# Kernel tuning notes

Measured on AMD Instinct MI355X. Metric: run time of the kernel, lower is better.

Reference implementation:

```python
import jax, jax.numpy as jnp
import numpy as np
from functools import reduce

# 2x2 beamsplitter gate (1/sqrt(2)) * [[1, i], [i, 1]]
BS_2x2 = (1.0 / np.sqrt(2.0)) * np.array([[1 + 0j, 0 + 1j], [0 + 1j, 1 + 0j]], dtype=np.complex64)


def _kron_phase_diag(a, b):
    """Diagonal vector of kron_i diag([e^{i a_i}, e^{i b_i}]) -> shape (2^n,) complex64.

    Mathematically identical to building the dense Kronecker diagonal matrix
    (as the original tf.linalg.LinearOperatorKronecker(...).to_dense()) and
    right-multiplying by it, since M @ diag(d) == M * d.
    """
    pairs = jnp.stack([jnp.exp(1j * a), jnp.exp(1j * b)], axis=1)  # (n, 2)
    n = pairs.shape[0]
    vec = pairs[0]
    for i in range(1, n):  # static small loop over qubits
        vec = jnp.kron(vec, pairs[i])
    return vec


def _bs_full(n):
    # Dense n-fold Kronecker product of the 2x2 beamsplitter, (2^n, 2^n) complex64
    return reduce(jnp.kron, [jnp.asarray(BS_2x2)] * n)


def setup_inputs() -> dict:
    key = jax.random.key(0)
    kx, ka, kb, kt, kp = jax.random.split(key, 5)
    n = 12
    N = 2 ** n
    batch = 64
    two_pi = 2.0 * np.pi
    return {
        "x": jax.random.normal(kx, (batch, 2, N), dtype=jnp.float32),
        "alphas": jax.random.uniform(ka, (n,), dtype=jnp.float32) * two_pi,
        "betas": jax.random.uniform(kb, (n,), dtype=jnp.float32) * two_pi,
        "thetas": jax.random.uniform(kt, (n,), dtype=jnp.float32) * two_pi,
        "phis": jax.random.uniform(kp, (n,), dtype=jnp.float32) * two_pi,
    }


def reference(x, alphas, betas, thetas, phis):
    n = alphas.shape[0]
    bs = _bs_full(n)                                   # (N, N) complex64
    d_in = _kron_phase_diag(alphas, betas)             # (N,)
    d_theta = _kron_phase_diag(thetas, jnp.zeros_like(thetas))
    d_phi = _kron_phase_diag(phis, jnp.zeros_like(phis))

    out = jax.lax.complex(x[:, 0, :], x[:, 1, :])      # (B, N) complex64
    out = (out * d_in) @ bs                            # input phase shifts + beamsplitter
    out = (out * d_theta) @ bs                         # theta shifts + beamsplitter
    out = out * d_phi                                  # final phi shifts
    return jnp.stack([out.real, out.imag], axis=1)     # (B, 2, N) float32
```

## Files before the change

kernel.cpp:

```cpp
#include <hip/hip_runtime.h>
#include <math.h>

#define NN 4096
#define BLK 512
#define EPT 8
#define PADSZ (NN + (NN >> 3))

__device__ __forceinline__ void cmul(float& ar, float& ai, float br, float bi) {
    float nr = ar * br - ai * bi;
    float ni = ar * bi + ai * br;
    ar = nr; ai = ni;
}

__device__ __forceinline__ void bfly_pair(float* vr, float* vi, int a, int b) {
    float ur = vr[a], ui = vi[a], wr = vr[b], wi = vi[b];
    vr[a] = ur - wi; vi[a] = ui + wr;
    vr[b] = wr - ui; vi[b] = wi + ur;
}

__device__ __forceinline__ void bfly3(float* vr, float* vi) {
    bfly_pair(vr, vi, 0, 1); bfly_pair(vr, vi, 2, 3); bfly_pair(vr, vi, 4, 5); bfly_pair(vr, vi, 6, 7);
    bfly_pair(vr, vi, 0, 2); bfly_pair(vr, vi, 1, 3); bfly_pair(vr, vi, 4, 6); bfly_pair(vr, vi, 5, 7);
    bfly_pair(vr, vi, 0, 4); bfly_pair(vr, vi, 1, 5); bfly_pair(vr, vi, 2, 6); bfly_pair(vr, vi, 3, 7);
}

template<int P>
__device__ __forceinline__ int jidx(int t, int r) {
    return ((t >> P) << (P + 3)) | (r << P) | (t & ((1 << P) - 1));
}

template<int PC, int PN, bool CROSS>
__device__ __forceinline__ void exchange(float2* buf, float* vr, float* vi, int t) {
    #pragma unroll
    for (int r = 0; r < EPT; ++r) {
        int j = jidx<PC>(t, r);
        buf[j + (j >> 3)] = make_float2(vr[r], vi[r]);
    }
    if (CROSS) { __syncthreads(); }
    else       { asm volatile("" ::: "memory"); }
    #pragma unroll
    for (int r = 0; r < EPT; ++r) {
        int j = jidx<PN>(t, r);
        float2 v = buf[j + (j >> 3)];
        vr[r] = v.x; vi[r] = v.y;
    }
}

__global__ __launch_bounds__(BLK) void qubit_layer_kernel(
    const float* __restrict__ x,
    const float* __restrict__ alphas, const float* __restrict__ betas,
    const float* __restrict__ thetas, const float* __restrict__ phis,
    float* __restrict__ out)
{
    __shared__ float2 B1[PADSZ];
    __shared__ float2 B2[PADSZ];
    __shared__ float2 tbl[6][64];

    const int t = threadIdx.x;
    const int b = blockIdx.x;

    if (t < 384) {
        int part = t >> 6, idx = t & 63, set = part >> 1, half = part & 1;
        float a = 0.f;
        #pragma unroll
        for (int m = 0; m < 6; ++m) {
            int q = half ? m : (6 + m);
            int bit = (idx >> (5 - m)) & 1;
            float av, bv;
            if (set == 0)      { av = alphas[q]; bv = betas[q]; }
            else if (set == 1) { av = thetas[q]; bv = 0.f; }
            else               { av = phis[q];   bv = 0.f; }
            a += bit ? bv : av;
        }
        float s, c;
        __sincosf(a, &s, &c);
        float sc = (set >= 1 && half == 0) ? (1.0f / 64.0f) : 1.0f;
        tbl[part][idx] = make_float2(c * sc, s * sc);
    }

    const float* xr = x + (size_t)b * 2 * NN;
    const float* xi = xr + NN;
    float vr[EPT], vi[EPT];
    {
        float4 a0 = ((const float4*)(xr + t * EPT))[0];
        float4 a1 = ((const float4*)(xr + t * EPT))[1];
        float4 c0 = ((const float4*)(xi + t * EPT))[0];
        float4 c1 = ((const float4*)(xi + t * EPT))[1];
        vr[0]=a0.x; vr[1]=a0.y; vr[2]=a0.z; vr[3]=a0.w; vr[4]=a1.x; vr[5]=a1.y; vr[6]=a1.z; vr[7]=a1.w;
        vi[0]=c0.x; vi[1]=c0.y; vi[2]=c0.z; vi[3]=c0.w; vi[4]=c1.x; vi[5]=c1.y; vi[6]=c1.z; vi[7]=c1.w;
    }
    __syncthreads();

    {
        float2 eh = tbl[1][t >> 3];
        const float4* elv = (const float4*)&tbl[0][(t & 7) << 3];
        #pragma unroll
        for (int k = 0; k < 4; ++k) {
            float4 e2 = elv[k];
            float er0 = e2.x, ei0 = e2.y, er1 = e2.z, ei1 = e2.w;
            cmul(er0, ei0, eh.x, eh.y);
            cmul(er1, ei1, eh.x, eh.y);
            cmul(vr[2*k],   vi[2*k],   er0, ei0);
            cmul(vr[2*k+1], vi[2*k+1], er1, ei1);
        }
    }

    bfly3(vr, vi);
    exchange<0, 3, false>(B1, vr, vi, t); bfly3(vr, vi);
    exchange<3, 6, false>(B1, vr, vi, t); bfly3(vr, vi);
    exchange<6, 9, true >(B1, vr, vi, t); bfly3(vr, vi);

    {
        float2 el = tbl[2][t & 63];
        #pragma unroll
        for (int r = 0; r < EPT; ++r) {
            float2 eh = tbl[3][(t >> 6) + (r << 3)];
            float er = el.x, ei = el.y;
            cmul(er, ei, eh.x, eh.y);
            cmul(vr[r], vi[r], er, ei);
        }
    }

    bfly3(vr, vi);
    exchange<9, 6, true >(B2, vr, vi, t); bfly3(vr, vi);
    exchange<6, 3, false>(B1, vr, vi, t); bfly3(vr, vi);
    exchange<3, 0, false>(B1, vr, vi, t); bfly3(vr, vi);

    {
        float2 eh = tbl[5][t >> 3];
        const float4* elv = (const float4*)&tbl[4][(t & 7) << 3];
        #pragma unroll
        for (int k = 0; k < 4; ++k) {
            float4 e2 = elv[k];
            float er0 = e2.x, ei0 = e2.y, er1 = e2.z, ei1 = e2.w;
            cmul(er0, ei0, eh.x, eh.y);
            cmul(er1, ei1, eh.x, eh.y);
            cmul(vr[2*k],   vi[2*k],   er0, ei0);
            cmul(vr[2*k+1], vi[2*k+1], er1, ei1);
        }
    }
    float* outr = out + (size_t)b * 2 * NN;
    float* outi = outr + NN;
    {
        ((float4*)(outr + t * EPT))[0] = make_float4(vr[0], vr[1], vr[2], vr[3]);
        ((float4*)(outr + t * EPT))[1] = make_float4(vr[4], vr[5], vr[6], vr[7]);
        ((float4*)(outi + t * EPT))[0] = make_float4(vi[0], vi[1], vi[2], vi[3]);
        ((float4*)(outi + t * EPT))[1] = make_float4(vi[4], vi[5], vi[6], vi[7]);
    }
}

extern "C" void kernel_launch(void* const* d_in, const int* in_sizes, int n_in,
                              void* d_out, int out_size, void* d_ws, size_t ws_size,
                              hipStream_t stream) {
    const float* x      = (const float*)d_in[0];
    const float* alphas = (const float*)d_in[1];
    const float* betas  = (const float*)d_in[2];
    const float* thetas = (const float*)d_in[3];
    const float* phis   = (const float*)d_in[4];
    float* out = (float*)d_out;

    const int batch = in_sizes[0] / (2 * NN);
    qubit_layer_kernel<<<batch, BLK, 0, stream>>>(x, alphas, betas, thetas, phis, out);
}
```

Before: 10.26 us.

## Replace LDS exchanges with wavefront shuffles and one XOR-swizzled transpose per transform

```diff
diff --git a/kernel.cpp b/kernel.cpp
--- a/kernel.cpp
+++ b/kernel.cpp
@@ -4,7 +4,6 @@
 #define NN 4096
 #define BLK 512
 #define EPT 8
-#define PADSZ (NN + (NN >> 3))
 
 __device__ __forceinline__ void cmul(float& ar, float& ai, float br, float bi) {
     float nr = ar * br - ai * bi;
@@ -24,26 +23,27 @@
     bfly_pair(vr, vi, 0, 4); bfly_pair(vr, vi, 1, 5); bfly_pair(vr, vi, 2, 6); bfly_pair(vr, vi, 3, 7);
 }
 
-template<int P>
-__device__ __forceinline__ int jidx(int t, int r) {
-    return ((t >> P) << (P + 3)) | (r << P) | (t & ((1 << P) - 1));
+__device__ __forceinline__ void shfl_stage(float* vr, float* vi, int mask) {
+    float pr[EPT], pi[EPT];
+    #pragma unroll
+    for (int r = 0; r < EPT; ++r) {
+        pr[r] = __shfl_xor(vr[r], mask);
+        pi[r] = __shfl_xor(vi[r], mask);
+    }
+    #pragma unroll
+    for (int r = 0; r < EPT; ++r) {
+        vr[r] -= pi[r];
+        vi[r] += pr[r];
+    }
 }
 
-template<int PC, int PN, bool CROSS>
-__device__ __forceinline__ void exchange(float2* buf, float* vr, float* vi, int t) {
-    #pragma unroll
-    for (int r = 0; r < EPT; ++r) {
-        int j = jidx<PC>(t, r);
-        buf[j + (j >> 3)] = make_float2(vr[r], vi[r]);
-    }
-    if (CROSS) { __syncthreads(); }
-    else       { asm volatile("" ::: "memory"); }
-    #pragma unroll
-    for (int r = 0; r < EPT; ++r) {
-        int j = jidx<PN>(t, r);
-        float2 v = buf[j + (j >> 3)];
-        vr[r] = v.x; vi[r] = v.y;
-    }
+__device__ __forceinline__ void shfl6(float* vr, float* vi) {
+    shfl_stage(vr, vi, 1);
+    shfl_stage(vr, vi, 2);
+    shfl_stage(vr, vi, 4);
+    shfl_stage(vr, vi, 8);
+    shfl_stage(vr, vi, 16);
+    shfl_stage(vr, vi, 32);
 }
 
 __global__ __launch_bounds__(BLK) void qubit_layer_kernel(
@@ -52,12 +52,21 @@
     const float* __restrict__ thetas, const float* __restrict__ phis,
     float* __restrict__ out)
 {
-    __shared__ float2 B1[PADSZ];
-    __shared__ float2 B2[PADSZ];
+    __shared__ float2 E1[NN];
+    __shared__ float2 E2[NN];
     __shared__ float2 tbl[6][64];
 
-    const int t = threadIdx.x;
-    const int b = blockIdx.x;
+    const int t   = threadIdx.x;
+    const int w   = t >> 6;
+    const int lam = t & 63;
+    const int b   = blockIdx.x;
+
+    const float* xr = x + (size_t)b * 2 * NN;
+    const float* xi = xr + NN;
+    float4 a0 = ((const float4*)(xr + t * EPT))[0];
+    float4 a1 = ((const float4*)(xr + t * EPT))[1];
+    float4 c0 = ((const float4*)(xi + t * EPT))[0];
+    float4 c1 = ((const float4*)(xi + t * EPT))[1];
 
     if (t < 384) {
         int part = t >> 6, idx = t & 63, set = part >> 1, half = part & 1;
@@ -78,22 +87,15 @@
         tbl[part][idx] = make_float2(c * sc, s * sc);
     }
 
-    const float* xr = x + (size_t)b * 2 * NN;
-    const float* xi = xr + NN;
     float vr[EPT], vi[EPT];
-    {
-        float4 a0 = ((const float4*)(xr + t * EPT))[0];
-        float4 a1 = ((const float4*)(xr + t * EPT))[1];
-        float4 c0 = ((const float4*)(xi + t * EPT))[0];
-        float4 c1 = ((const float4*)(xi + t * EPT))[1];
-        vr[0]=a0.x; vr[1]=a0.y; vr[2]=a0.z; vr[3]=a0.w; vr[4]=a1.x; vr[5]=a1.y; vr[6]=a1.z; vr[7]=a1.w;
-        vi[0]=c0.x; vi[1]=c0.y; vi[2]=c0.z; vi[3]=c0.w; vi[4]=c1.x; vi[5]=c1.y; vi[6]=c1.z; vi[7]=c1.w;
-    }
+    vr[0]=a0.x; vr[1]=a0.y; vr[2]=a0.z; vr[3]=a0.w; vr[4]=a1.x; vr[5]=a1.y; vr[6]=a1.z; vr[7]=a1.w;
+    vi[0]=c0.x; vi[1]=c0.y; vi[2]=c0.z; vi[3]=c0.w; vi[4]=c1.x; vi[5]=c1.y; vi[6]=c1.z; vi[7]=c1.w;
+
     __syncthreads();
 
     {
-        float2 eh = tbl[1][t >> 3];
-        const float4* elv = (const float4*)&tbl[0][(t & 7) << 3];
+        float2 eh = tbl[1][(w << 3) | (lam >> 3)];
+        const float4* elv = (const float4*)&tbl[0][(lam & 7) << 3];
         #pragma unroll
         for (int k = 0; k < 4; ++k) {
             float4 e2 = elv[k];
@@ -106,15 +108,25 @@
     }
 
     bfly3(vr, vi);
-    exchange<0, 3, false>(B1, vr, vi, t); bfly3(vr, vi);
-    exchange<3, 6, false>(B1, vr, vi, t); bfly3(vr, vi);
-    exchange<6, 9, true >(B1, vr, vi, t); bfly3(vr, vi);
+    shfl6(vr, vi);
+    {
+        #pragma unroll
+        for (int r = 0; r < EPT; ++r)
+            E1[(lam << 6) | (((w << 3) | r) ^ lam)] = make_float2(vr[r], vi[r]);
+        __syncthreads();
+        #pragma unroll
+        for (int r = 0; r < EPT; ++r) {
+            float2 v = E1[(lam << 6) | (((r << 3) | w) ^ lam)];
+            vr[r] = v.x; vi[r] = v.y;
+        }
+    }
+    bfly3(vr, vi);
 
     {
-        float2 el = tbl[2][t & 63];
+        float2 el = tbl[2][((lam & 7) << 3) | w];
         #pragma unroll
         for (int r = 0; r < EPT; ++r) {
-            float2 eh = tbl[3][(t >> 6) + (r << 3)];
+            float2 eh = tbl[3][(r << 3) | (lam >> 3)];
             float er = el.x, ei = el.y;
             cmul(er, ei, eh.x, eh.y);
             cmul(vr[r], vi[r], er, ei);
@@ -122,13 +134,23 @@
     }
 
     bfly3(vr, vi);
-    exchange<9, 6, true >(B2, vr, vi, t); bfly3(vr, vi);
-    exchange<6, 3, false>(B1, vr, vi, t); bfly3(vr, vi);
-    exchange<3, 0, false>(B1, vr, vi, t); bfly3(vr, vi);
+    shfl6(vr, vi);
+    {
+        #pragma unroll
+        for (int r = 0; r < EPT; ++r)
+            E2[(lam << 6) | (((r << 3) | w) ^ lam)] = make_float2(vr[r], vi[r]);
+        __syncthreads();
+        #pragma unroll
+        for (int r = 0; r < EPT; ++r) {
+            float2 v = E2[(lam << 6) | (((w << 3) | r) ^ lam)];
+            vr[r] = v.x; vi[r] = v.y;
+        }
+    }
+    bfly3(vr, vi);
 
     {
-        float2 eh = tbl[5][t >> 3];
-        const float4* elv = (const float4*)&tbl[4][(t & 7) << 3];
+        float2 eh = tbl[5][(w << 3) | (lam >> 3)];
+        const float4* elv = (const float4*)&tbl[4][(lam & 7) << 3];
         #pragma unroll
         for (int k = 0; k < 4; ++k) {
             float4 e2 = elv[k];
@@ -141,12 +163,10 @@
     }
     float* outr = out + (size_t)b * 2 * NN;
     float* outi = outr + NN;
-    {
-        ((float4*)(outr + t * EPT))[0] = make_float4(vr[0], vr[1], vr[2], vr[3]);
-        ((float4*)(outr + t * EPT))[1] = make_float4(vr[4], vr[5], vr[6], vr[7]);
-        ((float4*)(outi + t * EPT))[0] = make_float4(vi[0], vi[1], vi[2], vi[3]);
-        ((float4*)(outi + t * EPT))[1] = make_float4(vi[4], vi[5], vi[6], vi[7]);
-    }
+    ((float4*)(outr + t * EPT))[0] = make_float4(vr[0], vr[1], vr[2], vr[3]);
+    ((float4*)(outr + t * EPT))[1] = make_float4(vr[4], vr[5], vr[6], vr[7]);
+    ((float4*)(outi + t * EPT))[0] = make_float4(vi[0], vi[1], vi[2], vi[3]);
+    ((float4*)(outi + t * EPT))[1] = make_float4(vi[4], vi[5], vi[6], vi[7]);
 }
 
 extern "C" void kernel_launch(void* const* d_in, const int* in_sizes, int n_in,
```

Result: slower. 12.96 us (+26.3%).
